# Kernel tuning notes

Measured on AMD Instinct MI355X. Metric: run time of the kernel, lower is better.

## Reference

```python
import jax, jax.numpy as jnp
import numpy as np
from jax import lax

K = 5  # carafe kernel size


def conv2d(x, w, b=None, padding='SAME'):
    y = lax.conv_general_dilated(x, w, (1, 1), padding,
                                 dimension_numbers=('NHWC', 'HWIO', 'NHWC'))
    return y if b is None else y + b


def upsample2x(x):
    return jnp.repeat(jnp.repeat(x, 2, axis=1), 2, axis=2)


def carafe(coarse, kernel):
    # coarse: [B,H,W,C]; kernel: [B,2H,2W,K*K] predicted at fine resolution
    B, H, W, C = coarse.shape
    pad = K // 2
    p = jnp.pad(coarse, ((0, 0), (pad, pad), (pad, pad), (0, 0)))
    # [B,H,W,K*K,C] neighborhoods, row-major (di,dj) order
    patches = jnp.stack([p[:, di:di + H, dj:dj + W, :]
                         for di in range(K) for dj in range(K)], axis=3)
    # softmax-normalized reassembly weights; fine pixel (i,j) -> coarse (i//2,j//2)
    mask = jax.nn.softmax(kernel, axis=-1).reshape(B, H, 2, W, 2, K * K)
    out = jnp.einsum('bhxwyk,bhwkc->bhxwyc', mask, patches)
    return out.reshape(B, 2 * H, 2 * W, C)


def setup_inputs() -> dict:
    key = jax.random.key(0)
    ks = jax.random.split(key, 8)
    B, H, W = 4, 64, 64
    Cf, Cc, E, F = 128, 256, 64, 256
    s = lambda k, shape: jax.random.normal(k, shape, jnp.float32) * 0.05
    z = lambda n: jnp.zeros((n,), jnp.float32)
    return dict(
        fine=jax.random.normal(ks[0], (B, 2 * H, 2 * W, Cf), jnp.float32),
        coarse=jax.random.normal(ks[1], (B, H, W, Cc), jnp.float32),
        gate_w=s(ks[2], (1, 1, Cc, 1)), gate_b=z(1),
        ss_fine_w=s(ks[3], (1, 1, Cf, E)), ss_fine_b=z(E),
        ss_coarse_w=s(ks[4], (1, 1, Cc, E)),
        ss_content_w=s(ks[5], (3, 3, E, K * K)), ss_content_b=z(K * K),
        coarse_proj_w=s(ks[6], (1, 1, Cc, F)), coarse_proj_b=z(F),
        fine_proj_w=s(ks[7], (1, 1, F, F)), fine_proj_b=z(F),
    )


def reference(fine, coarse, gate_w, gate_b, ss_fine_w, ss_fine_b, ss_coarse_w,
              ss_content_w, ss_content_b, coarse_proj_w, coarse_proj_b,
              fine_proj_w, fine_proj_b):
    # gate branch: 1x1 conv + sigmoid on coarse, nearest-upsample to fine size
    gate = upsample2x(jax.nn.sigmoid(conv2d(coarse, gate_w, gate_b)))
    # SemiShift kernel prediction: shared 3x3 'content' conv on both embeddings
    f = conv2d(conv2d(fine, ss_fine_w, ss_fine_b), ss_content_w, ss_content_b)
    c = conv2d(conv2d(coarse, ss_coarse_w), ss_content_w, ss_content_b)
    kernel = f + upsample2x(c)  # [B,2H,2W,K*K]
    # CARAFE content-aware reassembly of coarse at fine resolution
    cu = carafe(coarse, kernel)
    c_out = conv2d(cu, coarse_proj_w, coarse_proj_b)
    # NOTE: faithful to source -- 'fine' projection is applied to the coarse output
    f_out = conv2d(c_out, fine_proj_w, fine_proj_b)
    return gate * f_out + (1.0 - gate) * c_out
```

## Files before the change

### kernel.cpp

```cpp
#include <hip/hip_runtime.h>
#include <math.h>

constexpr int Bb = 4, Hc = 64, Wc = 64, Cc = 256, Cf = 128, E = 64, KK = 25, F = 256;
constexpr int Hf = 128, Wf = 128;
constexpr int Nc = Bb * Hc * Wc;
constexpr int Nf = Bb * Hf * Wf;

typedef __attribute__((ext_vector_type(8))) short bf16x8;
typedef __attribute__((ext_vector_type(4))) float f32x4;

__device__ inline unsigned short f2b(float f) {
  union { float f; unsigned u; } v; v.f = f;
  return (unsigned short)((v.u + 0x7FFF + ((v.u >> 16) & 1)) >> 16);
}

__global__ __launch_bounds__(256) void prep_kernel(
    const float* __restrict__ W1, const float* __restrict__ W2,
    unsigned short* __restrict__ Wt1, unsigned short* __restrict__ Wt12,
    float* __restrict__ b12f, const float* __restrict__ b1,
    const float* __restrict__ b2,
    const float* __restrict__ fw, const float* __restrict__ cw,
    const float* __restrict__ cntw, unsigned short* __restrict__ Wtf,
    unsigned short* __restrict__ Wtc, unsigned short* __restrict__ Wtcnt,
    const float* __restrict__ coarse, const float* __restrict__ gw,
    const float* __restrict__ gb, float* __restrict__ gatec) {
  __shared__ __align__(16) char smem[64 * 72 * 2 * 2];
  int idx = blockIdx.x, t = threadIdx.x;

  if (idx < 16) {
    float (*tile)[65] = (float(*)[65])smem;
    int k0 = ((idx >> 2) & 3) * 64, n0 = (idx & 3) * 64;
    int r0 = t >> 6, c = t & 63;
    for (int r = r0; r < 64; r += 4)
      tile[r][c] = W1[(size_t)(k0 + r) * 256 + n0 + c];
    __syncthreads();
    for (int r = r0; r < 64; r += 4)
      Wt1[(size_t)(n0 + r) * 256 + k0 + c] = f2b(tile[c][r]);
  } else if (idx < 19) {
    int sec = idx - 16;
    if (sec == 0) {
      for (int i = t; i < 64 * 128; i += 256) {
        int n = i & 63, k = i >> 6;
        Wtf[n * 128 + k] = f2b(fw[k * 64 + n]);
      }
    } else if (sec == 1) {
      for (int i = t; i < 64 * 256; i += 256) {
        int n = i & 63, k = i >> 6;
        Wtc[n * 256 + k] = f2b(cw[k * 64 + n]);
      }
    } else {
      for (int i = t; i < 32 * 576; i += 256) {
        int n = i & 31, kk = i >> 5;
        Wtcnt[n * 576 + kk] = (n < 25) ? f2b(cntw[kk * 25 + n]) : (unsigned short)0;
      }
    }
  } else if (idx < 35) {
    unsigned short* a_s = (unsigned short*)smem;
    unsigned short* b_s = (unsigned short*)smem + 64 * 72;
    int sub = idx - 19;
    int nbase = (sub & 3) * 64, k0 = (sub >> 2) * 64;
    int wid = t >> 6, lane = t & 63;
    int lr = lane & 15, lg = lane >> 4;
    const f32x4 zero4 = {0.f, 0.f, 0.f, 0.f};
    f32x4 acc[4] = {zero4, zero4, zero4, zero4};

    for (int mc = 0; mc < 4; mc++) {
      for (int i = t; i < 64 * 16; i += 256) {
        int r = i >> 4, c4 = i & 15;
        float4 v = *(const float4*)&W1[(size_t)(k0 + r) * 256 + mc * 64 + c4 * 4];
        *(short4*)&a_s[r * 72 + c4 * 4] =
            make_short4((short)f2b(v.x), (short)f2b(v.y), (short)f2b(v.z), (short)f2b(v.w));
      }
      for (int i = t; i < 64 * 16; i += 256) {
        int m = i >> 4, n4 = i & 15;
        float4 v = *(const float4*)&W2[(size_t)(mc * 64 + m) * 256 + nbase + n4 * 4];
        b_s[(n4 * 4 + 0) * 72 + m] = f2b(v.x);
        b_s[(n4 * 4 + 1) * 72 + m] = f2b(v.y);
        b_s[(n4 * 4 + 2) * 72 + m] = f2b(v.z);
        b_s[(n4 * 4 + 3) * 72 + m] = f2b(v.w);
      }
      __syncthreads();
      #pragma unroll
      for (int kt = 0; kt < 2; kt++) {
        bf16x8 a = *(const bf16x8*)&a_s[(wid * 16 + lr) * 72 + kt * 32 + lg * 8];
        #pragma unroll
        for (int nt = 0; nt < 4; nt++) {
          bf16x8 bb = *(const bf16x8*)&b_s[(nt * 16 + lr) * 72 + kt * 32 + lg * 8];
          acc[nt] = __builtin_amdgcn_mfma_f32_16x16x32_bf16(a, bb, acc[nt], 0, 0, 0);
        }
      }
      __syncthreads();
    }
    #pragma unroll
    for (int nt = 0; nt < 4; nt++)
      #pragma unroll
      for (int r = 0; r < 4; r++)
        Wt12[(size_t)(nbase + nt * 16 + lr) * 256 + k0 + wid * 16 + lg * 4 + r] =
            f2b(acc[nt][r]);
  } else if (idx == 35) {
    int n = t;
    float acc = b2[n];
    #pragma unroll 8
    for (int m = 0; m < 256; m++) acc += b1[m] * W2[(size_t)m * 256 + n];
    b12f[n] = acc;
  } else {
    int w = t >> 6, lane = t & 63;
    int base = (idx - 36) * 64 + w * 16;
    const float4 wv = *(const float4*)(gw + lane * 4);
    float gb0 = gb[0];
    #pragma unroll
    for (int rnd = 0; rnd < 2; rnd++) {
      int p0 = base + rnd * 8;
      float a0, a1, a2, a3, a4, a5, a6, a7;
      {
        float4 v0 = *(const float4*)(coarse + (size_t)(p0 + 0) * 256 + lane * 4);
        float4 v1 = *(const float4*)(coarse + (size_t)(p0 + 1) * 256 + lane * 4);
        float4 v2 = *(const float4*)(coarse + (size_t)(p0 + 2) * 256 + lane * 4);
        float4 v3 = *(const float4*)(coarse + (size_t)(p0 + 3) * 256 + lane * 4);
        float4 v4 = *(const float4*)(coarse + (size_t)(p0 + 4) * 256 + lane * 4);
        float4 v5 = *(const float4*)(coarse + (size_t)(p0 + 5) * 256 + lane * 4);
        float4 v6 = *(const float4*)(coarse + (size_t)(p0 + 6) * 256 + lane * 4);
        float4 v7 = *(const float4*)(coarse + (size_t)(p0 + 7) * 256 + lane * 4);
        a0 = v0.x * wv.x + v0.y * wv.y + v0.z * wv.z + v0.w * wv.w;
        a1 = v1.x * wv.x + v1.y * wv.y + v1.z * wv.z + v1.w * wv.w;
        a2 = v2.x * wv.x + v2.y * wv.y + v2.z * wv.z + v2.w * wv.w;
        a3 = v3.x * wv.x + v3.y * wv.y + v3.z * wv.z + v3.w * wv.w;
        a4 = v4.x * wv.x + v4.y * wv.y + v4.z * wv.z + v4.w * wv.w;
        a5 = v5.x * wv.x + v5.y * wv.y + v5.z * wv.z + v5.w * wv.w;
        a6 = v6.x * wv.x + v6.y * wv.y + v6.z * wv.z + v6.w * wv.w;
        a7 = v7.x * wv.x + v7.y * wv.y + v7.z * wv.z + v7.w * wv.w;
      }
      #pragma unroll
      for (int off2 = 32; off2; off2 >>= 1) {
        a0 += __shfl_xor(a0, off2);
        a1 += __shfl_xor(a1, off2);
        a2 += __shfl_xor(a2, off2);
        a3 += __shfl_xor(a3, off2);
        a4 += __shfl_xor(a4, off2);
        a5 += __shfl_xor(a5, off2);
        a6 += __shfl_xor(a6, off2);
        a7 += __shfl_xor(a7, off2);
      }
      if (lane == 0) {
        gatec[p0 + 0] = 1.f / (1.f + expf(-(a0 + gb0)));
        gatec[p0 + 1] = 1.f / (1.f + expf(-(a1 + gb0)));
        gatec[p0 + 2] = 1.f / (1.f + expf(-(a2 + gb0)));
        gatec[p0 + 3] = 1.f / (1.f + expf(-(a3 + gb0)));
        gatec[p0 + 4] = 1.f / (1.f + expf(-(a4 + gb0)));
        gatec[p0 + 5] = 1.f / (1.f + expf(-(a5 + gb0)));
        gatec[p0 + 6] = 1.f / (1.f + expf(-(a6 + gb0)));
        gatec[p0 + 7] = 1.f / (1.f + expf(-(a7 + gb0)));
      }
    }
  }
}

template <int K>
__device__ inline void emb_body(const float* __restrict__ in,
                                const unsigned short* __restrict__ Wt,
                                const float* __restrict__ bias,
                                unsigned short* __restrict__ out, int pxb,
                                unsigned short* a_s) {
  constexpr int LDA = K + 8;
  int t = threadIdx.x;
  constexpr int KC = K / 4;
  for (int idx = t; idx < 64 * KC; idx += 256) {
    int px = idx / KC, kc = idx % KC;
    float4 v = *(const float4*)&in[(size_t)(pxb + px) * K + kc * 4];
    *(short4*)&a_s[px * LDA + kc * 4] =
        make_short4((short)f2b(v.x), (short)f2b(v.y), (short)f2b(v.z), (short)f2b(v.w));
  }
  __syncthreads();

  int wid = t >> 6, lane = t & 63;
  int lr = lane & 15, lg = lane >> 4;
  const f32x4 zero4 = {0.f, 0.f, 0.f, 0.f};
  f32x4 acc[4] = {zero4, zero4, zero4, zero4};

  #pragma unroll
  for (int kt = 0; kt < K / 32; kt++) {
    bf16x8 a = *(const bf16x8*)&a_s[(wid * 16 + lr) * LDA + kt * 32 + lg * 8];
    #pragma unroll
    for (int nt = 0; nt < 4; nt++) {
      bf16x8 bb = *(const bf16x8*)&Wt[(size_t)(nt * 16 + lr) * K + kt * 32 + lg * 8];
      acc[nt] = __builtin_amdgcn_mfma_f32_16x16x32_bf16(a, bb, acc[nt], 0, 0, 0);
    }
  }

  #pragma unroll
  for (int nt = 0; nt < 4; nt++) {
    int n = nt * 16 + lr;
    float bv = bias ? bias[n] : 0.f;
    #pragma unroll
    for (int r = 0; r < 4; r++) {
      int px = wid * 16 + lg * 4 + r;
      out[(size_t)(pxb + px) * 64 + n] = f2b(acc[nt][r] + bv);
    }
  }
}

__global__ __launch_bounds__(256) void emb_both_kernel(
    const float* __restrict__ fine, const unsigned short* __restrict__ Wtf,
    const float* __restrict__ fbias, unsigned short* __restrict__ femb,
    const float* __restrict__ coarse, const unsigned short* __restrict__ Wtc,
    unsigned short* __restrict__ cemb) {
  __shared__ __align__(16) unsigned short a_s[64 * 264];
  int idx = blockIdx.x;
  if (idx < Nf / 64) emb_body<128>(fine, Wtf, fbias, femb, idx * 64, a_s);
  else               emb_body<256>(coarse, Wtc, nullptr, cemb, (idx - Nf / 64) * 64, a_s);
}

__global__ __launch_bounds__(256) void content_both_kernel(
    const unsigned short* __restrict__ femb, const unsigned short* __restrict__ cemb,
    const unsigned short* __restrict__ Wtcnt, const float* __restrict__ cb,
    float* __restrict__ kff, float* __restrict__ kfc) {
  __shared__ __align__(16) unsigned short a_s[324 * 72];
  int idx = blockIdx.x, t = threadIdx.x;
  const unsigned short* emb;
  float* out;
  int b, i0, j0, Hd, Wd;
  if (idx < 256) {
    b = idx >> 6; int rem = idx & 63;
    i0 = (rem >> 3) * 16; j0 = (rem & 7) * 16; Hd = 128; Wd = 128;
    emb = femb; out = kff;
  } else {
    int i2 = idx - 256;
    b = i2 >> 4; int rem = i2 & 15;
    i0 = (rem >> 2) * 16; j0 = (rem & 3) * 16; Hd = 64; Wd = 64;
    emb = cemb; out = kfc;
  }

  for (int i = t; i < 324 * 16; i += 256) {
    int cell = i >> 4, ck = i & 15;
    int gi = i0 - 1 + cell / 18;
    int gj = j0 - 1 + cell % 18;
    short4 v = make_short4(0, 0, 0, 0);
    if (gi >= 0 && gi < Hd && gj >= 0 && gj < Wd)
      v = *(const short4*)&emb[(size_t)((b * Hd + gi) * Wd + gj) * 64 + ck * 4];
    *(short4*)&a_s[cell * 72 + ck * 4] = v;
  }
  __syncthreads();

  int wid = t >> 6, lane = t & 63;
  int lr = lane & 15, lg = lane >> 4;
  const f32x4 zero4 = {0.f, 0.f, 0.f, 0.f};
  f32x4 acc[4][2];
  #pragma unroll
  for (int mt = 0; mt < 4; mt++)
    #pragma unroll
    for (int nt = 0; nt < 2; nt++) acc[mt][nt] = zero4;

  #pragma unroll
  for (int nt = 0; nt < 2; nt++) {
    bf16x8 wb[9][2];
    #pragma unroll
    for (int tap = 0; tap < 9; tap++)
      #pragma unroll
      for (int kt = 0; kt < 2; kt++)
        wb[tap][kt] = *(const bf16x8*)&Wtcnt[(size_t)(nt * 16 + lr) * 576 + tap * 64 + kt * 32 + lg * 8];

    #pragma unroll
    for (int mt = 0; mt < 4; mt++) {
      int m = wid * 4 + mt;
      #pragma unroll
      for (int di = 0; di < 3; di++) {
        #pragma unroll
        for (int dj = 0; dj < 3; dj++) {
          int cell = (m + di) * 18 + (lr + dj);
          int tap = di * 3 + dj;
          #pragma unroll
          for (int kt = 0; kt < 2; kt++) {
            bf16x8 a = *(const bf16x8*)&a_s[cell * 72 + kt * 32 + lg * 8];
            acc[mt][nt] = __builtin_amdgcn_mfma_f32_16x16x32_bf16(a, wb[tap][kt], acc[mt][nt], 0, 0, 0);
          }
        }
      }
    }
  }

  #pragma unroll
  for (int mt = 0; mt < 4; mt++) {
    int m = wid * 4 + mt;
    int gi = i0 + m;
    #pragma unroll
    for (int nt = 0; nt < 2; nt++) {
      int ch = nt * 16 + lr;
      if (ch < 25) {
        float bv = cb[ch];
        #pragma unroll
        for (int r = 0; r < 4; r++) {
          int gj = j0 + lg * 4 + r;
          out[(size_t)((b * Hd + gi) * Wd + gj) * 25 + ch] = acc[mt][nt][r] + bv;
        }
      }
    }
  }
}

__global__ __launch_bounds__(256) void carafe_kernel(
    const float* __restrict__ coarse, const float* __restrict__ kff,
    const float* __restrict__ kfc, unsigned short* __restrict__ cu_g) {
  __shared__ __align__(16) unsigned short buf[256 * 72];
  __shared__ __align__(16) unsigned short m_ext[64 * 72];
  unsigned short* win_t = buf;
  unsigned short* cu_s  = buf;

  int t = threadIdx.x;
  int b = blockIdx.z;
  int i0 = blockIdx.y * 8, j0 = blockIdx.x * 8;
  int hw0 = (i0 >> 1) - 2, ww0 = (j0 >> 1) - 2;

  {
    #pragma unroll
    for (int p0 = 0; p0 < 64; p0 += 4) {
      unsigned short vals[4];
      #pragma unroll
      for (int q = 0; q < 4; q++) {
        int p = p0 + q;
        int h = hw0 + (p >> 3), w = ww0 + (p & 7);
        float v = 0.f;
        if (h >= 0 && h < 64 && w >= 0 && w < 64)
          v = coarse[(size_t)((b * 64 + h) * 64 + w) * 256 + t];
        vals[q] = f2b(v);
      }
      *(short4*)&win_t[t * 72 + p0] =
          make_short4((short)vals[0], (short)vals[1], (short)vals[2], (short)vals[3]);
    }
  }
  if (t < 64) {
    int ti = t >> 3, tj = t & 7;
    int i = i0 + ti, j = j0 + tj;
    size_t fpx = (size_t)((b * 128 + i) * 128 + j);
    size_t cpx = (size_t)((b * 64 + (i >> 1)) * 64 + (j >> 1));
    float v[25];
    float mx = -1e30f;
    #pragma unroll
    for (int m = 0; m < 25; m++) {
      v[m] = kff[fpx * 25 + m] + kfc[cpx * 25 + m];
      mx = fmaxf(mx, v[m]);
    }
    float s = 0.f;
    #pragma unroll
    for (int m = 0; m < 25; m++) { v[m] = expf(v[m] - mx); s += v[m]; }
    float inv = 1.f / s;
    unsigned* row32 = (unsigned*)&m_ext[t * 72];
    #pragma unroll
    for (int q = 0; q < 36; q++) row32[q] = 0;
    int wib = ti >> 1, wjb = tj >> 1;
    #pragma unroll
    for (int di = 0; di < 5; di++)
      #pragma unroll
      for (int dj = 0; dj < 5; dj++)
        m_ext[t * 72 + (wib + di) * 8 + (wjb + dj)] = f2b(v[di * 5 + dj] * inv);
  }
  __syncthreads();

  int wid = t >> 6, lane = t & 63;
  int lr = lane & 15, lg = lane >> 4;
  const f32x4 zero4 = {0.f, 0.f, 0.f, 0.f};

  f32x4 acc0[4][4];
  #pragma unroll
  for (int mi = 0; mi < 4; mi++)
    #pragma unroll
    for (int ni = 0; ni < 4; ni++) acc0[mi][ni] = zero4;
  #pragma unroll
  for (int kt = 0; kt < 2; kt++) {
    bf16x8 am[4];
    #pragma unroll
    for (int mi = 0; mi < 4; mi++)
      am[mi] = *(const bf16x8*)&m_ext[(mi * 16 + lr) * 72 + kt * 32 + lg * 8];
    #pragma unroll
    for (int ni = 0; ni < 4; ni++) {
      bf16x8 bb = *(const bf16x8*)&win_t[(size_t)(wid * 64 + ni * 16 + lr) * 72 + kt * 32 + lg * 8];
      #pragma unroll
      for (int mi = 0; mi < 4; mi++)
        acc0[mi][ni] = __builtin_amdgcn_mfma_f32_16x16x32_bf16(am[mi], bb, acc0[mi][ni], 0, 0, 0);
    }
  }
  __syncthreads();

  #pragma unroll
  for (int mi = 0; mi < 4; mi++)
    #pragma unroll
    for (int ni = 0; ni < 4; ni++)
      #pragma unroll
      for (int r = 0; r < 4; r++)
        cu_s[(mi * 16 + lg * 4 + r) * 264 + wid * 64 + ni * 16 + lr] = f2b(acc0[mi][ni][r]);
  __syncthreads();

  for (int c = t; c < 2048; c += 256) {
    int p = c >> 5, off = (c & 31) << 3;
    int gi = i0 + (p >> 3), gj = j0 + (p & 7);
    bf16x8 v = *(const bf16x8*)&cu_s[p * 264 + off];
    *(bf16x8*)&cu_g[(size_t)((b * 128 + gi) * 128 + gj) * 256 + off] = v;
  }
}

__global__ __launch_bounds__(256, 2) void proj_kernel(
    const unsigned short* __restrict__ cu_g, const float* __restrict__ gatec,
    const unsigned short* __restrict__ Wt1, const float* __restrict__ b1,
    const unsigned short* __restrict__ Wt12, const float* __restrict__ b12,
    float* __restrict__ out) {
  __shared__ __align__(16) unsigned short a_s[2][64 * 264];
  __shared__ float g_s[2][32];
  int t = threadIdx.x;
  int bid = blockIdx.x;
  int cg = bid >> 8;
  int g  = bid & 255;
  int wid = t >> 6, lane = t & 63;
  int lr = lane & 15, lg = lane >> 4;
  int n0 = cg * 64 + wid * 16;

  bf16x8 wb1[8], wb12[8];
  #pragma unroll
  for (int kt = 0; kt < 8; kt++) {
    size_t wrow = (size_t)(n0 + lr) * 256 + kt * 32 + lg * 8;
    wb1[kt]  = *(const bf16x8*)&Wt1[wrow];
    wb12[kt] = *(const bf16x8*)&Wt12[wrow];
  }
  float b1v  = b1[n0 + lr];
  float b12v = b12[n0 + lr];

  {
    size_t m0 = (size_t)g * 256;
    for (int c = t; c < 2048; c += 256) {
      int row = c >> 5, off = (c & 31) << 3;
      *(bf16x8*)&a_s[0][row * 264 + off] = *(const bf16x8*)&cu_g[(m0 + row) * 256 + off];
    }
    if (t < 32) {
      int b_ = (int)(m0 >> 14), ii = (int)((m0 >> 7) & 127), j0 = (int)(m0 & 127);
      g_s[0][t] = gatec[(size_t)(b_ * 64 + (ii >> 1)) * 64 + (j0 >> 1) + t];
    }
  }
  __syncthreads();

  const f32x4 zero4 = {0.f, 0.f, 0.f, 0.f};

  for (int it = 0; it < 4; ++it) {
    int cur = it & 1, nxt = cur ^ 1;
    size_t m0i = (size_t)(g * 4 + it) * 64;

    bf16x8 pf[8];
    float gpf = 0.f;
    if (it < 3) {
      size_t m0n = m0i + 64;
      #pragma unroll
      for (int q = 0; q < 8; q++) {
        int c = t + q * 256;
        int row = c >> 5, off = (c & 31) << 3;
        pf[q] = *(const bf16x8*)&cu_g[(m0n + row) * 256 + off];
      }
      if (t < 32) {
        int b_ = (int)(m0n >> 14), ii = (int)((m0n >> 7) & 127), j0 = (int)(m0n & 127);
        gpf = gatec[(size_t)(b_ * 64 + (ii >> 1)) * 64 + (j0 >> 1) + t];
      }
    }

    f32x4 accc[4] = {zero4, zero4, zero4, zero4};
    f32x4 accf[4] = {zero4, zero4, zero4, zero4};
    #pragma unroll
    for (int kt = 0; kt < 8; kt++) {
      #pragma unroll
      for (int mi = 0; mi < 4; mi++) {
        bf16x8 a = *(const bf16x8*)&a_s[cur][(mi * 16 + lr) * 264 + kt * 32 + lg * 8];
        accc[mi] = __builtin_amdgcn_mfma_f32_16x16x32_bf16(a, wb1[kt],  accc[mi], 0, 0, 0);
        accf[mi] = __builtin_amdgcn_mfma_f32_16x16x32_bf16(a, wb12[kt], accf[mi], 0, 0, 0);
      }
    }

    if (it < 3) {
      #pragma unroll
      for (int q = 0; q < 8; q++) {
        int c = t + q * 256;
        int row = c >> 5, off = (c & 31) << 3;
        *(bf16x8*)&a_s[nxt][row * 264 + off] = pf[q];
      }
      if (t < 32) g_s[nxt][t] = gpf;
    }

    #pragma unroll
    for (int mi = 0; mi < 4; mi++) {
      #pragma unroll
      for (int r = 0; r < 4; r++) {
        int row = mi * 16 + lg * 4 + r;
        float gg = g_s[cur][row >> 1];
        float f_out = accf[mi][r] + b12v;
        float c_out = accc[mi][r] + b1v;
        out[(m0i + row) * 256 + n0 + lr] = gg * f_out + (1.f - gg) * c_out;
      }
    }

    if (it < 3) __syncthreads();
  }
}

extern "C" void kernel_launch(void* const* d_in, const int* in_sizes, int n_in,
                              void* d_out, int out_size, void* d_ws, size_t ws_size,
                              hipStream_t stream) {
  const float* fine        = (const float*)d_in[0];
  const float* coarse      = (const float*)d_in[1];
  const float* gate_w      = (const float*)d_in[2];
  const float* gate_b      = (const float*)d_in[3];
  const float* ss_fine_w   = (const float*)d_in[4];
  const float* ss_fine_b   = (const float*)d_in[5];
  const float* ss_coarse_w = (const float*)d_in[6];
  const float* ss_content_w= (const float*)d_in[7];
  const float* ss_content_b= (const float*)d_in[8];
  const float* W1          = (const float*)d_in[9];
  const float* b1          = (const float*)d_in[10];
  const float* W2          = (const float*)d_in[11];
  const float* b2          = (const float*)d_in[12];
  float* out = (float*)d_out;

  char* ws = (char*)d_ws;
  size_t off = 0;
  float* gatec = (float*)(ws + off); off += 131072;
  unsigned short* femb = (unsigned short*)(ws + off); off += (size_t)Nf * 64 * 2;
  unsigned short* cemb = (unsigned short*)(ws + off); off += (size_t)Nc * 64 * 2;
  float* kff   = (float*)(ws + off); off += (size_t)Nf * 25 * 4;
  float* kfc   = (float*)(ws + off); off += (size_t)Nc * 25 * 4;
  unsigned short* Wt1 = (unsigned short*)(ws + off); off += 65536 * 2;
  unsigned short* Wtf = (unsigned short*)(ws + off); off += 64 * 128 * 2;
  unsigned short* Wtc = (unsigned short*)(ws + off); off += 64 * 256 * 2;
  unsigned short* Wtcnt = (unsigned short*)(ws + off); off += 32 * 576 * 2;
  unsigned short* Wt12 = (unsigned short*)(ws + off); off += 65536 * 2;
  float* b12f = (float*)(ws + off); off += 1024;
  unsigned short* cu_g = (unsigned short*)(ws + off); off += (size_t)Nf * 256 * 2;

  prep_kernel<<<36 + 256, 256, 0, stream>>>(
      W1, W2, Wt1, Wt12, b12f, b1, b2, ss_fine_w, ss_coarse_w, ss_content_w,
      Wtf, Wtc, Wtcnt, coarse, gate_w, gate_b, gatec);
  emb_both_kernel<<<Nf / 64 + Nc / 64, 256, 0, stream>>>(
      fine, Wtf, ss_fine_b, femb, coarse, Wtc, cemb);
  content_both_kernel<<<256 + 64, 256, 0, stream>>>(
      femb, cemb, Wtcnt, ss_content_b, kff, kfc);
  carafe_kernel<<<dim3(Wf / 8, Hf / 8, Bb), 256, 0, stream>>>(coarse, kff, kfc, cu_g);
  proj_kernel<<<1024, 256, 0, stream>>>(cu_g, gatec, Wt1, b1, Wt12, b12f, out);
}
```

Measured before the change: 132.1 us.

## Split weight prep and fuse independent prep work into embedding kernel

Moves the small embedding and content weight transposes into a tiny, fully parallel prep kernel. The projection weight prep, the W1·W2 product, the folded bias and the gate computation become extra blocks of the embedding kernel, so they run alongside the embedding GEMMs instead of in a separate serial launch. This shortens the critical path of the long single-block prep loops and leaves the launch count unchanged. The cost is a larger combined kernel with heterogeneous blocks, and the bias reduction is split over four partial accumulators.

Result: faster. 114.1 us (-13.7%).

```diff
diff --git a/kernel.cpp b/kernel.cpp
--- a/kernel.cpp
+++ b/kernel.cpp
@@ -14,50 +14,103 @@
   return (unsigned short)((v.u + 0x7FFF + ((v.u >> 16) & 1)) >> 16);
 }
 
-__global__ __launch_bounds__(256) void prep_kernel(
+__global__ __launch_bounds__(256) void prepA_kernel(
+    const float* __restrict__ fw, const float* __restrict__ cw,
+    const float* __restrict__ cntw, unsigned short* __restrict__ Wtf,
+    unsigned short* __restrict__ Wtc, unsigned short* __restrict__ Wtcnt) {
+  int gid = blockIdx.x * 256 + threadIdx.x;
+  if (gid < 8192) {
+    int i = gid;
+    int n = i & 63, k = i >> 6;
+    Wtf[n * 128 + k] = f2b(fw[i]);
+  } else if (gid < 8192 + 16384) {
+    int i = gid - 8192;
+    int n = i & 63, k = i >> 6;
+    Wtc[n * 256 + k] = f2b(cw[i]);
+  } else if (gid < 8192 + 16384 + 18432) {
+    int i = gid - 8192 - 16384;
+    int n = i & 31, kk = i >> 5;
+    Wtcnt[n * 576 + kk] = (n < 25) ? f2b(cntw[kk * 25 + n]) : (unsigned short)0;
+  }
+}
+
+template <int K>
+__device__ inline void emb_body(const float* __restrict__ in,
+                                const unsigned short* __restrict__ Wt,
+                                const float* __restrict__ bias,
+                                unsigned short* __restrict__ out, int pxb,
+                                unsigned short* a_s) {
+  constexpr int LDA = K + 8;
+  int t = threadIdx.x;
+  constexpr int KC = K / 4;
+  for (int idx = t; idx < 64 * KC; idx += 256) {
+    int px = idx / KC, kc = idx % KC;
+    float4 v = *(const float4*)&in[(size_t)(pxb + px) * K + kc * 4];
+    *(short4*)&a_s[px * LDA + kc * 4] =
+        make_short4((short)f2b(v.x), (short)f2b(v.y), (short)f2b(v.z), (short)f2b(v.w));
+  }
+  __syncthreads();
+
+  int wid = t >> 6, lane = t & 63;
+  int lr = lane & 15, lg = lane >> 4;
+  const f32x4 zero4 = {0.f, 0.f, 0.f, 0.f};
+  f32x4 acc[4] = {zero4, zero4, zero4, zero4};
+
+  #pragma unroll
+  for (int kt = 0; kt < K / 32; kt++) {
+    bf16x8 a = *(const bf16x8*)&a_s[(wid * 16 + lr) * LDA + kt * 32 + lg * 8];
+    #pragma unroll
+    for (int nt = 0; nt < 4; nt++) {
+      bf16x8 bb = *(const bf16x8*)&Wt[(size_t)(nt * 16 + lr) * K + kt * 32 + lg * 8];
+      acc[nt] = __builtin_amdgcn_mfma_f32_16x16x32_bf16(a, bb, acc[nt], 0, 0, 0);
+    }
+  }
+
+  #pragma unroll
+  for (int nt = 0; nt < 4; nt++) {
+    int n = nt * 16 + lr;
+    float bv = bias ? bias[n] : 0.f;
+    #pragma unroll
+    for (int r = 0; r < 4; r++) {
+      int px = wid * 16 + lg * 4 + r;
+      out[(size_t)(pxb + px) * 64 + n] = f2b(acc[nt][r] + bv);
+    }
+  }
+}
+
+__global__ __launch_bounds__(256) void emb_prepB_kernel(
+    const float* __restrict__ fine, const unsigned short* __restrict__ Wtf,
+    const float* __restrict__ fbias, unsigned short* __restrict__ femb,
+    const float* __restrict__ coarse, const unsigned short* __restrict__ Wtc,
+    unsigned short* __restrict__ cemb,
     const float* __restrict__ W1, const float* __restrict__ W2,
     unsigned short* __restrict__ Wt1, unsigned short* __restrict__ Wt12,
     float* __restrict__ b12f, const float* __restrict__ b1,
-    const float* __restrict__ b2,
-    const float* __restrict__ fw, const float* __restrict__ cw,
-    const float* __restrict__ cntw, unsigned short* __restrict__ Wtf,
-    unsigned short* __restrict__ Wtc, unsigned short* __restrict__ Wtcnt,
-    const float* __restrict__ coarse, const float* __restrict__ gw,
+    const float* __restrict__ b2, const float* __restrict__ gw,
     const float* __restrict__ gb, float* __restrict__ gatec) {
-  __shared__ __align__(16) char smem[64 * 72 * 2 * 2];
+  __shared__ __align__(16) unsigned short pool[64 * 264];
   int idx = blockIdx.x, t = threadIdx.x;
 
-  if (idx < 16) {
-    float (*tile)[65] = (float(*)[65])smem;
-    int k0 = ((idx >> 2) & 3) * 64, n0 = (idx & 3) * 64;
+  if (idx < Nf / 64) {
+    emb_body<128>(fine, Wtf, fbias, femb, idx * 64, pool);
+  } else if (idx < 1280) {
+    emb_body<256>(coarse, Wtc, nullptr, cemb, (idx - Nf / 64) * 64, pool);
+  } else if (idx < 1296) {
+    float (*tile)[65] = (float(*)[65])pool;
+    int sub = idx - 1280;
+    int k0 = ((sub >> 2) & 3) * 64, n0 = (sub & 3) * 64;
     int r0 = t >> 6, c = t & 63;
+    #pragma unroll
     for (int r = r0; r < 64; r += 4)
       tile[r][c] = W1[(size_t)(k0 + r) * 256 + n0 + c];
     __syncthreads();
+    #pragma unroll
     for (int r = r0; r < 64; r += 4)
       Wt1[(size_t)(n0 + r) * 256 + k0 + c] = f2b(tile[c][r]);
-  } else if (idx < 19) {
-    int sec = idx - 16;
-    if (sec == 0) {
-      for (int i = t; i < 64 * 128; i += 256) {
-        int n = i & 63, k = i >> 6;
-        Wtf[n * 128 + k] = f2b(fw[k * 64 + n]);
-      }
-    } else if (sec == 1) {
-      for (int i = t; i < 64 * 256; i += 256) {
-        int n = i & 63, k = i >> 6;
-        Wtc[n * 256 + k] = f2b(cw[k * 64 + n]);
-      }
-    } else {
-      for (int i = t; i < 32 * 576; i += 256) {
-        int n = i & 31, kk = i >> 5;
-        Wtcnt[n * 576 + kk] = (n < 25) ? f2b(cntw[kk * 25 + n]) : (unsigned short)0;
-      }
-    }
-  } else if (idx < 35) {
-    unsigned short* a_s = (unsigned short*)smem;
-    unsigned short* b_s = (unsigned short*)smem + 64 * 72;
-    int sub = idx - 19;
+  } else if (idx < 1312) {
+    unsigned short* a_s = pool;
+    unsigned short* b_s = pool + 64 * 72;
+    int sub = idx - 1296;
     int nbase = (sub & 3) * 64, k0 = (sub >> 2) * 64;
     int wid = t >> 6, lane = t & 63;
     int lr = lane & 15, lg = lane >> 4;
@@ -97,15 +150,20 @@
       for (int r = 0; r < 4; r++)
         Wt12[(size_t)(nbase + nt * 16 + lr) * 256 + k0 + wid * 16 + lg * 4 + r] =
             f2b(acc[nt][r]);
-  } else if (idx == 35) {
+  } else if (idx == 1312) {
     int n = t;
-    float acc = b2[n];
-    #pragma unroll 8
-    for (int m = 0; m < 256; m++) acc += b1[m] * W2[(size_t)m * 256 + n];
-    b12f[n] = acc;
+    float a0 = 0.f, a1 = 0.f, a2 = 0.f, a3 = 0.f;
+    #pragma unroll 4
+    for (int m = 0; m < 256; m += 4) {
+      a0 += b1[m + 0] * W2[(size_t)(m + 0) * 256 + n];
+      a1 += b1[m + 1] * W2[(size_t)(m + 1) * 256 + n];
+      a2 += b1[m + 2] * W2[(size_t)(m + 2) * 256 + n];
+      a3 += b1[m + 3] * W2[(size_t)(m + 3) * 256 + n];
+    }
+    b12f[n] = (a0 + a1) + (a2 + a3) + b2[n];
   } else {
     int w = t >> 6, lane = t & 63;
-    int base = (idx - 36) * 64 + w * 16;
+    int base = (idx - 1313) * 64 + w * 16;
     const float4 wv = *(const float4*)(gw + lane * 4);
     float gb0 = gb[0];
     #pragma unroll
@@ -155,61 +213,6 @@
   }
 }
 
-template <int K>
-__device__ inline void emb_body(const float* __restrict__ in,
-                                const unsigned short* __restrict__ Wt,
-                                const float* __restrict__ bias,
-                                unsigned short* __restrict__ out, int pxb,
-                                unsigned short* a_s) {
-  constexpr int LDA = K + 8;
-  int t = threadIdx.x;
-  constexpr int KC = K / 4;
-  for (int idx = t; idx < 64 * KC; idx += 256) {
-    int px = idx / KC, kc = idx % KC;
-    float4 v = *(const float4*)&in[(size_t)(pxb + px) * K + kc * 4];
-    *(short4*)&a_s[px * LDA + kc * 4] =
-        make_short4((short)f2b(v.x), (short)f2b(v.y), (short)f2b(v.z), (short)f2b(v.w));
-  }
-  __syncthreads();
-
-  int wid = t >> 6, lane = t & 63;
-  int lr = lane & 15, lg = lane >> 4;
-  const f32x4 zero4 = {0.f, 0.f, 0.f, 0.f};
-  f32x4 acc[4] = {zero4, zero4, zero4, zero4};
-
-  #pragma unroll
-  for (int kt = 0; kt < K / 32; kt++) {
-    bf16x8 a = *(const bf16x8*)&a_s[(wid * 16 + lr) * LDA + kt * 32 + lg * 8];
-    #pragma unroll
-    for (int nt = 0; nt < 4; nt++) {
-      bf16x8 bb = *(const bf16x8*)&Wt[(size_t)(nt * 16 + lr) * K + kt * 32 + lg * 8];
-      acc[nt] = __builtin_amdgcn_mfma_f32_16x16x32_bf16(a, bb, acc[nt], 0, 0, 0);
-    }
-  }
-
-  #pragma unroll
-  for (int nt = 0; nt < 4; nt++) {
-    int n = nt * 16 + lr;
-    float bv = bias ? bias[n] : 0.f;
-    #pragma unroll
-    for (int r = 0; r < 4; r++) {
-      int px = wid * 16 + lg * 4 + r;
-      out[(size_t)(pxb + px) * 64 + n] = f2b(acc[nt][r] + bv);
-    }
-  }
-}
-
-__global__ __launch_bounds__(256) void emb_both_kernel(
-    const float* __restrict__ fine, const unsigned short* __restrict__ Wtf,
-    const float* __restrict__ fbias, unsigned short* __restrict__ femb,
-    const float* __restrict__ coarse, const unsigned short* __restrict__ Wtc,
-    unsigned short* __restrict__ cemb) {
-  __shared__ __align__(16) unsigned short a_s[64 * 264];
-  int idx = blockIdx.x;
-  if (idx < Nf / 64) emb_body<128>(fine, Wtf, fbias, femb, idx * 64, a_s);
-  else               emb_body<256>(coarse, Wtc, nullptr, cemb, (idx - Nf / 64) * 64, a_s);
-}
-
 __global__ __launch_bounds__(256) void content_both_kernel(
     const unsigned short* __restrict__ femb, const unsigned short* __restrict__ cemb,
     const unsigned short* __restrict__ Wtcnt, const float* __restrict__ cb,
@@ -528,11 +531,11 @@
   float* b12f = (float*)(ws + off); off += 1024;
   unsigned short* cu_g = (unsigned short*)(ws + off); off += (size_t)Nf * 256 * 2;
 
-  prep_kernel<<<36 + 256, 256, 0, stream>>>(
-      W1, W2, Wt1, Wt12, b12f, b1, b2, ss_fine_w, ss_coarse_w, ss_content_w,
-      Wtf, Wtc, Wtcnt, coarse, gate_w, gate_b, gatec);
-  emb_both_kernel<<<Nf / 64 + Nc / 64, 256, 0, stream>>>(
-      fine, Wtf, ss_fine_b, femb, coarse, Wtc, cemb);
+  prepA_kernel<<<168, 256, 0, stream>>>(ss_fine_w, ss_coarse_w, ss_content_w,
+                                        Wtf, Wtc, Wtcnt);
+  emb_prepB_kernel<<<1569, 256, 0, stream>>>(
+      fine, Wtf, ss_fine_b, femb, coarse, Wtc, cemb,
+      W1, W2, Wt1, Wt12, b12f, b1, b2, gate_w, gate_b, gatec);
   content_both_kernel<<<256 + 64, 256, 0, stream>>>(
       femb, cemb, Wtcnt, ss_content_b, kff, kfc);
   carafe_kernel<<<dim3(Wf / 8, Hf / 8, Bb), 256, 0, stream>>>(coarse, kff, kfc, cu_g);
```
